# Optimization experiments

Measured on AMD Instinct MI355X. Metric: run time of the kernel, lower is better.

## Reference

```python
import jax, jax.numpy as jnp
import numpy as np

N = 50000        # n_nodes
E = 800000       # n_edges (avg degree 16)
H = 64           # hidden_size
ALPHA = 0.5      # CRF alpha
BETA = 0.5       # CRF beta
N_LAYER = 2      # args.crf_layer
GAMMA = 0.2      # LeakyReLU negative slope


def setup_inputs() -> dict:
    key = jax.random.key(0)
    k = jax.random.split(key, 5)
    emb = jax.random.normal(k[0], (N, H), jnp.float32)
    W_fc = jax.random.normal(k[1], (H, H), jnp.float32) / np.sqrt(H)
    attn_fc_w = jax.random.normal(k[2], (1, 2 * H), jnp.float32) / np.sqrt(2 * H)
    src = jax.random.randint(k[3], (E,), 0, N, dtype=jnp.int32)
    dst = jax.random.randint(k[4], (E,), 0, N, dtype=jnp.int32)
    return {"emb": emb, "W_fc": W_fc, "attn_fc_w": attn_fc_w, "src": src, "dst": dst}


def _segment_softmax(e, dst, n):
    # softmax over incoming edges of each destination node (DGL mailbox softmax)
    m = jax.ops.segment_max(e, dst, num_segments=n)
    m = jnp.where(jnp.isfinite(m), m, 0.0)  # nodes with no in-edges
    ex = jnp.exp(e - m[dst])
    denom = jax.ops.segment_sum(ex, dst, num_segments=n)
    return ex / jnp.maximum(denom[dst], 1e-16)


def reference(emb, W_fc, attn_fc_w, src, dst):
    # attn_fc(concat(z_src, z_dst)) split into two per-node projections
    a_src = attn_fc_w[0, :H]
    a_dst = attn_fc_w[0, H:]
    h = emb
    e = None
    for _ in range(N_LAYER):
        z = h @ W_fc.T                              # [N, H] emb_attn
        e = (z @ a_src)[src] + (z @ a_dst)[dst]     # [E] edge logits
        e = jnp.where(e > 0, e, GAMMA * e)          # LeakyReLU(gamma)
        att = _segment_softmax(e, dst, N)           # [E]
        crf = jax.ops.segment_sum(att[:, None] * h[src], dst, num_segments=N)  # [N, H]
        h = (ALPHA * emb + BETA * crf) / (ALPHA + BETA)
    # training loss (is_train=True); reuses last layer's edge logits e
    loss_a = jnp.sum((h - emb) ** 2, axis=-1)                     # [N]
    att = _segment_softmax(e, dst, N)
    diff = jnp.sqrt(jnp.sum((h[dst] - h[src]) ** 2, axis=-1) + 1e-12)  # [E] L2 norm
    loss_b = jax.ops.segment_sum(att * diff, dst, num_segments=N)  # [N]
    loss = jnp.mean(ALPHA * loss_a + BETA * loss_b)
    return h, loss
```

## Files before the change

kernel.cpp:

```cpp
#include <hip/hip_runtime.h>

#define NNODES 50000
#define NEDGES 800000
#define HDIM 64
#define CAP 64
#define GAMMA 0.2f
#define SCAN_B 256
#define SCAN_NB ((NNODES + SCAN_B - 1) / SCAN_B)
#define LOSS_GRID 2048
#define NPART 8
#define NODES_PER_PART ((NNODES + NPART - 1) / NPART)
#define FILL_SLICES 192
#define E4 (NEDGES / 4)
#define CHUNK ((E4 + FILL_SLICES - 1) / FILL_SLICES)

typedef unsigned short u16;
typedef unsigned int u32;

__device__ __forceinline__ u16 f2bf(float f) {
    u32 u = __float_as_uint(f);
    u32 r = (u + 0x7FFFu + ((u >> 16) & 1u)) >> 16;
    return (u16)r;
}
__device__ __forceinline__ float bflo(u32 u) { return __uint_as_float(u << 16); }
__device__ __forceinline__ float bfhi(u32 u) { return __uint_as_float(u & 0xFFFF0000u); }

__device__ __forceinline__ float wave_sum(float v) {
    #pragma unroll
    for (int off = 32; off; off >>= 1) v += __shfl_xor(v, off, 64);
    return v;
}
__device__ __forceinline__ float wave_max(float v) {
    #pragma unroll
    for (int off = 32; off; off >>= 1) v = fmaxf(v, __shfl_xor(v, off, 64));
    return v;
}
__device__ __forceinline__ int wave_sum_i(int v) {
    #pragma unroll
    for (int off = 32; off; off >>= 1) v += __shfl_xor(v, off, 64);
    return v;
}
__device__ __forceinline__ float group8_sum(float v) {
    v += __shfl_xor(v, 1, 64);
    v += __shfl_xor(v, 2, 64);
    v += __shfl_xor(v, 4, 64);
    return v;
}

__global__ void k_wswd(const float* __restrict__ Wfc, const float* __restrict__ attn,
                       float* __restrict__ ws, float* __restrict__ wd) {
    int t = threadIdx.x;
    int k = t & 63;
    const float* av = attn + ((t >= 64) ? HDIM : 0);
    float s = 0.f;
    for (int j = 0; j < HDIM; ++j) s += Wfc[j * HDIM + k] * av[j];
    if (t < 64) ws[k] = s; else wd[k] = s;
}

__global__ __launch_bounds__(256) void k_fillx(const int4* __restrict__ src4,
                                               const int4* __restrict__ dst4,
                                               int* __restrict__ cursor,
                                               u16* __restrict__ padded,
                                               const float* __restrict__ emb,
                                               const float* __restrict__ ws,
                                               const float* __restrict__ wd,
                                               u16* __restrict__ emb_bf,
                                               float* __restrict__ zs, float* __restrict__ zd) {
    if (blockIdx.x < NPART * FILL_SLICES) {
        const int part = blockIdx.x & (NPART - 1);
        const int slice = blockIdx.x >> 3;
        const int lo = slice * CHUNK;
        const int hi = min(lo + CHUNK, E4);
        const int plo = part * NODES_PER_PART;
        const int phi = plo + NODES_PER_PART;
        for (int i = lo + threadIdx.x; i < hi; i += 256) {
            int4 s = src4[i];
            int4 d = dst4[i];
            if (d.x >= plo && d.x < phi) { int p0 = atomicAdd(&cursor[d.x], 1); if (p0 < CAP) padded[d.x * CAP + p0] = (u16)s.x; }
            if (d.y >= plo && d.y < phi) { int p1 = atomicAdd(&cursor[d.y], 1); if (p1 < CAP) padded[d.y * CAP + p1] = (u16)s.y; }
            if (d.z >= plo && d.z < phi) { int p2 = atomicAdd(&cursor[d.z], 1); if (p2 < CAP) padded[d.z * CAP + p2] = (u16)s.z; }
            if (d.w >= plo && d.w < phi) { int p3 = atomicAdd(&cursor[d.w], 1); if (p3 < CAP) padded[d.w * CAP + p3] = (u16)s.w; }
        }
    }
    int tid = blockIdx.x * blockDim.x + threadIdx.x;
    int wid = tid >> 6;
    int lane = tid & 63;
    if (wid < NNODES) {
        float v = emb[wid * HDIM + lane];
        emb_bf[wid * HDIM + lane] = f2bf(v);
        float a = wave_sum(v * ws[lane]);
        float b = wave_sum(v * wd[lane]);
        if (lane == 0) { zs[wid] = a; zd[wid] = b; }
    }
}

__global__ __launch_bounds__(SCAN_B) void k_scan1(const int* __restrict__ deg,
                                                  int* __restrict__ blockSums) {
    int t = threadIdx.x;
    int idx = blockIdx.x * SCAN_B + t;
    int v = (idx < NNODES) ? min(deg[idx], CAP) : 0;
    int ws = wave_sum_i(v);
    __shared__ int part[4];
    if ((t & 63) == 0) part[t >> 6] = ws;
    __syncthreads();
    if (t == 0) blockSums[blockIdx.x] = part[0] + part[1] + part[2] + part[3];
}

__global__ __launch_bounds__(SCAN_B) void k_scan2(int* __restrict__ blockSums,
                                                  int* __restrict__ blockOffs) {
    __shared__ int s[SCAN_B];
    int t = threadIdx.x;
    int v = (t < SCAN_NB) ? blockSums[t] : 0;
    s[t] = v;
    __syncthreads();
    for (int off = 1; off < SCAN_B; off <<= 1) {
        int x = (t >= off) ? s[t - off] : 0;
        __syncthreads();
        s[t] += x;
        __syncthreads();
    }
    if (t < SCAN_NB) blockOffs[t] = s[t] - v;
}

__global__ __launch_bounds__(SCAN_B) void k_scan3(const int* __restrict__ deg,
                                                  const int* __restrict__ blockOffs,
                                                  int* __restrict__ row_ptr) {
    __shared__ int s[SCAN_B];
    int t = threadIdx.x;
    int idx = blockIdx.x * SCAN_B + t;
    int v = (idx < NNODES) ? min(deg[idx], CAP) : 0;
    s[t] = v;
    __syncthreads();
    for (int off = 1; off < SCAN_B; off <<= 1) {
        int x = (t >= off) ? s[t - off] : 0;
        __syncthreads();
        s[t] += x;
        __syncthreads();
    }
    if (idx < NNODES) {
        int excl = s[t] - v + blockOffs[blockIdx.x];
        row_ptr[idx] = excl;
        if (idx == NNODES - 1) row_ptr[NNODES] = excl + v;
    }
}

template <bool STORE_ATT, bool COMPUTE_Z, bool WRITE_F32, bool STORE_LA, bool COMPACT>
__global__ __launch_bounds__(256) void k_layer(const u16* __restrict__ hbf_in,
                                               const float* __restrict__ emb,
                                               const int* __restrict__ deg,
                                               const int* __restrict__ row_ptr,
                                               const u16* __restrict__ padded,
                                               const float* __restrict__ zs,
                                               const float* __restrict__ zd,
                                               float* __restrict__ att_csr,
                                               u16* __restrict__ csr_c,
                                               u16* __restrict__ dmap_c,
                                               float* __restrict__ h_out,
                                               u16* __restrict__ hbf_out,
                                               const float* __restrict__ ws,
                                               const float* __restrict__ wd,
                                               float* __restrict__ zs_out,
                                               float* __restrict__ zd_out,
                                               float* __restrict__ la) {
    int wid = (blockIdx.x * blockDim.x + threadIdx.x) >> 6;
    int lane = threadIdx.x & 63;
    if (wid >= NNODES) return;
    int ne = min(deg[wid], CAP);
    int s0 = 0;
    if (STORE_ATT || COMPACT) s0 = row_ptr[wid];
    float zdn = zd[wid];
    const int sub8 = lane >> 3, q8 = lane & 7;
    float acc[8];
    #pragma unroll
    for (int i = 0; i < 8; ++i) acc[i] = 0.f;

    int s = 0; float e = -INFINITY;
    bool valid = lane < ne;
    if (valid) {
        s = padded[wid * CAP + lane];
        float z = zs[s] + zdn;
        e = z > 0.f ? z : GAMMA * z;
    }
    float m = wave_max(e);
    float ex = valid ? __expf(e - m) : 0.f;
    float dsum = wave_sum(ex);
    float inv = 1.f / fmaxf(dsum, 1e-16f);
    if (STORE_ATT && valid) att_csr[s0 + lane] = ex * inv;
    if (COMPACT && valid) {
        csr_c[s0 + lane] = (u16)s;
        dmap_c[s0 + lane] = (u16)wid;
    }
    for (int j = 0; j < ne; j += 16) {
        int ja = j + sub8, jb = j + 8 + sub8;
        float wa = __shfl(ex, ja, 64);
        float wb = __shfl(ex, jb, 64);
        int ta = __shfl(s, ja, 64);
        int tb = __shfl(s, jb, 64);
        const uint4 ra = *(const uint4*)&hbf_in[(size_t)ta * HDIM + 8 * q8];
        const uint4 rb = *(const uint4*)&hbf_in[(size_t)tb * HDIM + 8 * q8];
        acc[0] += wa * bflo(ra.x) + wb * bflo(rb.x);
        acc[1] += wa * bfhi(ra.x) + wb * bfhi(rb.x);
        acc[2] += wa * bflo(ra.y) + wb * bflo(rb.y);
        acc[3] += wa * bfhi(ra.y) + wb * bfhi(rb.y);
        acc[4] += wa * bflo(ra.z) + wb * bflo(rb.z);
        acc[5] += wa * bfhi(ra.z) + wb * bfhi(rb.z);
        acc[6] += wa * bflo(ra.w) + wb * bflo(rb.w);
        acc[7] += wa * bfhi(ra.w) + wb * bfhi(rb.w);
    }
    #pragma unroll
    for (int off = 8; off <= 32; off <<= 1) {
        #pragma unroll
        for (int i = 0; i < 8; ++i) acc[i] += __shfl_xor(acc[i], off, 64);
    }
    float hv[8];
    #pragma unroll
    for (int i = 0; i < 8; ++i) hv[i] = 0.f;
    float lap = 0.f;
    if (sub8 == 0) {
        const float4 e0 = *(const float4*)&emb[(size_t)wid * HDIM + 8 * q8];
        const float4 e1 = *(const float4*)&emb[(size_t)wid * HDIM + 8 * q8 + 4];
        hv[0] = 0.5f * (e0.x + acc[0] * inv);
        hv[1] = 0.5f * (e0.y + acc[1] * inv);
        hv[2] = 0.5f * (e0.z + acc[2] * inv);
        hv[3] = 0.5f * (e0.w + acc[3] * inv);
        hv[4] = 0.5f * (e1.x + acc[4] * inv);
        hv[5] = 0.5f * (e1.y + acc[5] * inv);
        hv[6] = 0.5f * (e1.z + acc[6] * inv);
        hv[7] = 0.5f * (e1.w + acc[7] * inv);
        if (WRITE_F32) {
            *(float4*)&h_out[(size_t)wid * HDIM + 8 * q8]     = make_float4(hv[0], hv[1], hv[2], hv[3]);
            *(float4*)&h_out[(size_t)wid * HDIM + 8 * q8 + 4] = make_float4(hv[4], hv[5], hv[6], hv[7]);
        }
        uint4 o;
        o.x = (u32)f2bf(hv[0]) | ((u32)f2bf(hv[1]) << 16);
        o.y = (u32)f2bf(hv[2]) | ((u32)f2bf(hv[3]) << 16);
        o.z = (u32)f2bf(hv[4]) | ((u32)f2bf(hv[5]) << 16);
        o.w = (u32)f2bf(hv[6]) | ((u32)f2bf(hv[7]) << 16);
        *(uint4*)&hbf_out[(size_t)wid * HDIM + 8 * q8] = o;
        if (STORE_LA) {
            float d0 = hv[0] - e0.x, d1 = hv[1] - e0.y, d2 = hv[2] - e0.z, d3 = hv[3] - e0.w;
            float d4 = hv[4] - e1.x, d5 = hv[5] - e1.y, d6 = hv[6] - e1.z, d7 = hv[7] - e1.w;
            lap = d0 * d0 + d1 * d1 + d2 * d2 + d3 * d3 +
                  d4 * d4 + d5 * d5 + d6 * d6 + d7 * d7;
        }
    }
    if (STORE_LA) {
        float lsum = wave_sum(lap);
        if (lane == 0) la[wid] = lsum;
    }
    if (COMPUTE_Z) {
        float pa = 0.f, pb = 0.f;
        if (sub8 == 0) {
            const float4 w0 = *(const float4*)&ws[8 * q8];
            const float4 w1 = *(const float4*)&ws[8 * q8 + 4];
            const float4 d0 = *(const float4*)&wd[8 * q8];
            const float4 d1 = *(const float4*)&wd[8 * q8 + 4];
            pa = hv[0] * w0.x + hv[1] * w0.y + hv[2] * w0.z + hv[3] * w0.w +
                 hv[4] * w1.x + hv[5] * w1.y + hv[6] * w1.z + hv[7] * w1.w;
            pb = hv[0] * d0.x + hv[1] * d0.y + hv[2] * d0.z + hv[3] * d0.w +
                 hv[4] * d1.x + hv[5] * d1.y + hv[6] * d1.z + hv[7] * d1.w;
        }
        float a = wave_sum(pa);
        float b = wave_sum(pb);
        if (lane == 0) { zs_out[wid] = a; zd_out[wid] = b; }
    }
}

__global__ __launch_bounds__(256) void k_loss(const float* __restrict__ la,
                                              const u16* __restrict__ hbf,
                                              const u16* __restrict__ csr_src,
                                              const u16* __restrict__ dst_map,
                                              const float* __restrict__ att_csr,
                                              float* __restrict__ acc) {
    const int lane = threadIdx.x & 63;
    const int wib = threadIdx.x >> 6;
    const int gtid = blockIdx.x * blockDim.x + threadIdx.x;
    const int nthreads = gridDim.x * blockDim.x;
    const int gw = gtid >> 6;
    const int nwaves = nthreads >> 6;
    const int sub8 = lane >> 3, q8 = lane & 7;
    float lb = 0.f;

    for (int i = gtid; i < NNODES / 4; i += nthreads) {
        const float4 v = *(const float4*)&la[i * 4];
        lb += 0.5f * (v.x + v.y + v.z + v.w);
    }
    if ((NNODES & 3) != 0 && gtid < (NNODES & 3)) lb += 0.5f * la[(NNODES & ~3) + gtid];

    for (int g = gw; g < NEDGES / 16; g += nwaves) {
        int e0 = g * 16 + sub8;
        int e1 = e0 + 8;
        int s0i = csr_src[e0], d0i = dst_map[e0];
        int s1i = csr_src[e1], d1i = dst_map[e1];
        const uint4 rs0 = *(const uint4*)&hbf[(size_t)s0i * HDIM + 8 * q8];
        const uint4 rd0 = *(const uint4*)&hbf[(size_t)d0i * HDIM + 8 * q8];
        const uint4 rs1 = *(const uint4*)&hbf[(size_t)s1i * HDIM + 8 * q8];
        const uint4 rd1 = *(const uint4*)&hbf[(size_t)d1i * HDIM + 8 * q8];
        float a0 = bflo(rd0.x) - bflo(rs0.x), a1 = bfhi(rd0.x) - bfhi(rs0.x);
        float a2 = bflo(rd0.y) - bflo(rs0.y), a3 = bfhi(rd0.y) - bfhi(rs0.y);
        float a4 = bflo(rd0.z) - bflo(rs0.z), a5 = bfhi(rd0.z) - bfhi(rs0.z);
        float a6 = bflo(rd0.w) - bflo(rs0.w), a7 = bfhi(rd0.w) - bfhi(rs0.w);
        float b0 = bflo(rd1.x) - bflo(rs1.x), b1 = bfhi(rd1.x) - bfhi(rs1.x);
        float b2 = bflo(rd1.y) - bflo(rs1.y), b3 = bfhi(rd1.y) - bfhi(rs1.y);
        float b4 = bflo(rd1.z) - bflo(rs1.z), b5 = bfhi(rd1.z) - bfhi(rs1.z);
        float b6 = bflo(rd1.w) - bflo(rs1.w), b7 = bfhi(rd1.w) - bfhi(rs1.w);
        float ss0 = group8_sum(a0 * a0 + a1 * a1 + a2 * a2 + a3 * a3 +
                               a4 * a4 + a5 * a5 + a6 * a6 + a7 * a7);
        float ss1 = group8_sum(b0 * b0 + b1 * b1 + b2 * b2 + b3 * b3 +
                               b4 * b4 + b5 * b5 + b6 * b6 + b7 * b7);
        if (q8 == 0)
            lb += 0.5f * (att_csr[e0] * sqrtf(ss0 + 1e-12f) +
                          att_csr[e1] * sqrtf(ss1 + 1e-12f));
    }
    lb = wave_sum(lb);
    __shared__ float part[4];
    if (lane == 0) part[wib] = lb;
    __syncthreads();
    if (threadIdx.x == 0)
        atomicAdd(acc, part[0] + part[1] + part[2] + part[3]);
}

__global__ void k_finalize(const float* __restrict__ acc, float* __restrict__ out_loss) {
    out_loss[0] = acc[0] / (float)NNODES;
}

extern "C" void kernel_launch(void* const* d_in, const int* in_sizes, int n_in,
                              void* d_out, int out_size, void* d_ws, size_t ws_size,
                              hipStream_t stream) {
    const float* emb  = (const float*)d_in[0];
    const float* Wfc  = (const float*)d_in[1];
    const float* attn = (const float*)d_in[2];
    const int*   src  = (const int*)d_in[3];
    const int*   dst  = (const int*)d_in[4];
    float* out = (float*)d_out;

    char* p = (char*)d_ws;
    int*   cursor  = (int*)p;   p += (size_t)NNODES * 4;
    float* lossAcc = (float*)p; p += 256;
    int*   row_ptr = (int*)p;   p += (size_t)(NNODES + 1) * 4;
    int*   bsums   = (int*)p;   p += (size_t)SCAN_NB * 4;
    int*   boffs   = (int*)p;   p += (size_t)SCAN_NB * 4;
    float* wsv     = (float*)p; p += 64 * 4;
    float* wdv     = (float*)p; p += 64 * 4;
    float* zs0     = (float*)p; p += (size_t)NNODES * 4;
    float* zd0     = (float*)p; p += (size_t)NNODES * 4;
    float* zs1     = (float*)p; p += (size_t)NNODES * 4;
    float* zd1     = (float*)p; p += (size_t)NNODES * 4;
    float* laArr   = (float*)p; p += (size_t)NNODES * 4;
    float* att_csr = (float*)p; p += (size_t)NEDGES * 4;
    p = (char*)(((size_t)p + 255) & ~(size_t)255);
    u16*   padded  = (u16*)p;   p += (size_t)NNODES * CAP * 2;
    u16*   csr_src = (u16*)p;   p += (size_t)NEDGES * 2;
    u16*   dst_map = (u16*)p;   p += (size_t)NEDGES * 2;
    u16*   emb_bf  = (u16*)p;   p += (size_t)NNODES * HDIM * 2;
    u16*   h1_bf   = (u16*)p;   p += (size_t)NNODES * HDIM * 2;
    u16*   out_bf  = (u16*)p;   p += (size_t)NNODES * HDIM * 2;

    hipMemsetAsync(cursor, 0, (size_t)NNODES * 4 + 256, stream);

    const int NB = (NNODES + 3) / 4;

    k_wswd<<<1, 128, 0, stream>>>(Wfc, attn, wsv, wdv);
    k_fillx<<<NB, 256, 0, stream>>>((const int4*)src, (const int4*)dst, cursor, padded,
                                    emb, wsv, wdv, emb_bf, zs0, zd0);
    k_scan1<<<SCAN_NB, SCAN_B, 0, stream>>>(cursor, bsums);
    k_scan2<<<1, SCAN_B, 0, stream>>>(bsums, boffs);
    k_scan3<<<SCAN_NB, SCAN_B, 0, stream>>>(cursor, boffs, row_ptr);

    k_layer<false, true, false, false, true><<<NB, 256, 0, stream>>>(
        emb_bf, emb, cursor, row_ptr, padded, zs0, zd0,
        att_csr, csr_src, dst_map, out , h1_bf, wsv, wdv, zs1, zd1, laArr);
    k_layer<true, false, true, true, false><<<NB, 256, 0, stream>>>(
        h1_bf, emb, cursor, row_ptr, padded, zs1, zd1,
        att_csr, csr_src, dst_map, out, out_bf, wsv, wdv, zs0, zd0, laArr);

    k_loss<<<LOSS_GRID, 256, 0, stream>>>(laArr, out_bf, csr_src, dst_map, att_csr, lossAcc);
    k_finalize<<<1, 1, 0, stream>>>(lossAcc, out + (size_t)NNODES * HDIM);
}
```

Baseline: 231.0 us.

## Bucket edges by destination partition before scattering into padded adjacency

Building the padded adjacency used to read the full src/dst edge arrays once per each of 8 destination partitions, with most lanes filtering edges out. Now a bucketing kernel reads the edges once and packs (src,dst) pairs into per-wave, per-partition regions using ballot/popcount ranking. A scatter kernel then does the atomic inserts, keeping partition = blockIdx&7, so each partition's atomics stay on a fixed group of blocks. The emb bf16 conversion and z projections move into a fused scan1 kernel. This trades the redundant edge reads for an extra 3.2 MB intermediate write/read and one more kernel launch.

```diff
diff --git a/kernel.cpp b/kernel.cpp
--- a/kernel.cpp
+++ b/kernel.cpp
@@ -9,13 +9,15 @@
 #define SCAN_NB ((NNODES + SCAN_B - 1) / SCAN_B)
 #define LOSS_GRID 2048
 #define NPART 8
-#define NODES_PER_PART ((NNODES + NPART - 1) / NPART)
-#define FILL_SLICES 192
+#define PART_DIV 6272
 #define E4 (NEDGES / 4)
-#define CHUNK ((E4 + FILL_SLICES - 1) / FILL_SLICES)
+#define NWAVES_B1 512
+#define CHUNK_W ((E4 + NWAVES_B1 - 1) / NWAVES_B1)
+#define BCAP 512
 
 typedef unsigned short u16;
 typedef unsigned int u32;
+typedef unsigned long long u64;
 
 __device__ __forceinline__ u16 f2bf(float f) {
     u32 u = __float_as_uint(f);
@@ -57,30 +59,83 @@
     if (t < 64) ws[k] = s; else wd[k] = s;
 }
 
-__global__ __launch_bounds__(256) void k_fillx(const int4* __restrict__ src4,
-                                               const int4* __restrict__ dst4,
-                                               int* __restrict__ cursor,
-                                               u16* __restrict__ padded,
-                                               const float* __restrict__ emb,
-                                               const float* __restrict__ ws,
-                                               const float* __restrict__ wd,
-                                               u16* __restrict__ emb_bf,
-                                               float* __restrict__ zs, float* __restrict__ zd) {
-    if (blockIdx.x < NPART * FILL_SLICES) {
-        const int part = blockIdx.x & (NPART - 1);
-        const int slice = blockIdx.x >> 3;
-        const int lo = slice * CHUNK;
-        const int hi = min(lo + CHUNK, E4);
-        const int plo = part * NODES_PER_PART;
-        const int phi = plo + NODES_PER_PART;
-        for (int i = lo + threadIdx.x; i < hi; i += 256) {
-            int4 s = src4[i];
-            int4 d = dst4[i];
-            if (d.x >= plo && d.x < phi) { int p0 = atomicAdd(&cursor[d.x], 1); if (p0 < CAP) padded[d.x * CAP + p0] = (u16)s.x; }
-            if (d.y >= plo && d.y < phi) { int p1 = atomicAdd(&cursor[d.y], 1); if (p1 < CAP) padded[d.y * CAP + p1] = (u16)s.y; }
-            if (d.z >= plo && d.z < phi) { int p2 = atomicAdd(&cursor[d.z], 1); if (p2 < CAP) padded[d.z * CAP + p2] = (u16)s.z; }
-            if (d.w >= plo && d.w < phi) { int p3 = atomicAdd(&cursor[d.w], 1); if (p3 < CAP) padded[d.w * CAP + p3] = (u16)s.w; }
+__global__ __launch_bounds__(256) void k_bucket(const int4* __restrict__ src4,
+                                                const int4* __restrict__ dst4,
+                                                u32* __restrict__ region,
+                                                int* __restrict__ cnt_out) {
+    const int wid = (blockIdx.x * blockDim.x + threadIdx.x) >> 6;
+    const int lane = threadIdx.x & 63;
+    const u64 below = ((lane == 63) ? ~0ull : ((1ull << (lane + 1)) - 1)) >> 1;
+    const int lo = wid * CHUNK_W;
+    const int hi = min(lo + CHUNK_W, E4);
+    int cur[NPART];
+    #pragma unroll
+    for (int p = 0; p < NPART; ++p) cur[p] = 0;
+
+    for (int base = lo; base < hi; base += 64) {
+        int i = base + lane;
+        bool have = i < hi;
+        int4 s4 = have ? src4[i] : make_int4(0, 0, 0, 0);
+        int4 d4 = have ? dst4[i] : make_int4(0, 0, 0, 0);
+        #pragma unroll
+        for (int k = 0; k < 4; ++k) {
+            int s = (k == 0) ? s4.x : (k == 1) ? s4.y : (k == 2) ? s4.z : s4.w;
+            int d = (k == 0) ? d4.x : (k == 1) ? d4.y : (k == 2) ? d4.z : d4.w;
+            int part = have ? (d / PART_DIV) : NPART;
+            u32 v = (u32)s | ((u32)d << 16);
+            #pragma unroll
+            for (int p = 0; p < NPART; ++p) {
+                u64 m = __ballot(part == p);
+                if (m == 0ull) continue;
+                if (part == p) {
+                    int rank = __popcll(m & below);
+                    int pos = cur[p] + rank;
+                    if (pos < BCAP) region[((size_t)wid * NPART + p) * BCAP + pos] = v;
+                }
+                cur[p] += __popcll(m);
+            }
         }
+    }
+    #pragma unroll
+    for (int p = 0; p < NPART; ++p)
+        if (lane == p) cnt_out[wid * NPART + p] = min(cur[p], BCAP);
+}
+
+__global__ __launch_bounds__(256) void k_scatter(const u32* __restrict__ region,
+                                                 const int* __restrict__ cnt,
+                                                 int* __restrict__ cursor,
+                                                 u16* __restrict__ padded) {
+    const int part = blockIdx.x & (NPART - 1);
+    const int j = blockIdx.x >> 3;
+    for (int w = j; w < NWAVES_B1; w += 64) {
+        int n = cnt[w * NPART + part];
+        const u32* base = &region[((size_t)w * NPART + part) * BCAP];
+        for (int i = threadIdx.x; i < n; i += 256) {
+            u32 v = base[i];
+            int d = (int)(v >> 16);
+            int s = (int)(v & 0xFFFFu);
+            int pos = atomicAdd(&cursor[d], 1);
+            if (pos < CAP) padded[(size_t)d * CAP + pos] = (u16)s;
+        }
+    }
+}
+
+__global__ __launch_bounds__(256) void k_scan1z(const int* __restrict__ deg,
+                                                int* __restrict__ blockSums,
+                                                const float* __restrict__ emb,
+                                                const float* __restrict__ ws,
+                                                const float* __restrict__ wd,
+                                                u16* __restrict__ emb_bf,
+                                                float* __restrict__ zs, float* __restrict__ zd) {
+    int t = threadIdx.x;
+    if (blockIdx.x < SCAN_NB) {
+        int idx = blockIdx.x * SCAN_B + t;
+        int v = (idx < NNODES) ? min(deg[idx], CAP) : 0;
+        int wsum = wave_sum_i(v);
+        __shared__ int part[4];
+        if ((t & 63) == 0) part[t >> 6] = wsum;
+        __syncthreads();
+        if (t == 0) blockSums[blockIdx.x] = part[0] + part[1] + part[2] + part[3];
     }
     int tid = blockIdx.x * blockDim.x + threadIdx.x;
     int wid = tid >> 6;
@@ -92,18 +147,6 @@
         float b = wave_sum(v * wd[lane]);
         if (lane == 0) { zs[wid] = a; zd[wid] = b; }
     }
-}
-
-__global__ __launch_bounds__(SCAN_B) void k_scan1(const int* __restrict__ deg,
-                                                  int* __restrict__ blockSums) {
-    int t = threadIdx.x;
-    int idx = blockIdx.x * SCAN_B + t;
-    int v = (idx < NNODES) ? min(deg[idx], CAP) : 0;
-    int ws = wave_sum_i(v);
-    __shared__ int part[4];
-    if ((t & 63) == 0) part[t >> 6] = ws;
-    __syncthreads();
-    if (t == 0) blockSums[blockIdx.x] = part[0] + part[1] + part[2] + part[3];
 }
 
 __global__ __launch_bounds__(SCAN_B) void k_scan2(int* __restrict__ blockSums,
@@ -177,7 +220,7 @@
     int s = 0; float e = -INFINITY;
     bool valid = lane < ne;
     if (valid) {
-        s = padded[wid * CAP + lane];
+        s = padded[(size_t)wid * CAP + lane];
         float z = zs[s] + zdn;
         e = z > 0.f ? z : GAMMA * z;
     }
@@ -340,6 +383,7 @@
     int*   row_ptr = (int*)p;   p += (size_t)(NNODES + 1) * 4;
     int*   bsums   = (int*)p;   p += (size_t)SCAN_NB * 4;
     int*   boffs   = (int*)p;   p += (size_t)SCAN_NB * 4;
+    int*   bcnt    = (int*)p;   p += (size_t)NWAVES_B1 * NPART * 4;
     float* wsv     = (float*)p; p += 64 * 4;
     float* wdv     = (float*)p; p += 64 * 4;
     float* zs0     = (float*)p; p += (size_t)NNODES * 4;
@@ -349,6 +393,7 @@
     float* laArr   = (float*)p; p += (size_t)NNODES * 4;
     float* att_csr = (float*)p; p += (size_t)NEDGES * 4;
     p = (char*)(((size_t)p + 255) & ~(size_t)255);
+    u32*   region  = (u32*)p;   p += (size_t)NWAVES_B1 * NPART * BCAP * 4;
     u16*   padded  = (u16*)p;   p += (size_t)NNODES * CAP * 2;
     u16*   csr_src = (u16*)p;   p += (size_t)NEDGES * 2;
     u16*   dst_map = (u16*)p;   p += (size_t)NEDGES * 2;
@@ -361,9 +406,10 @@
     const int NB = (NNODES + 3) / 4;
 
     k_wswd<<<1, 128, 0, stream>>>(Wfc, attn, wsv, wdv);
-    k_fillx<<<NB, 256, 0, stream>>>((const int4*)src, (const int4*)dst, cursor, padded,
-                                    emb, wsv, wdv, emb_bf, zs0, zd0);
-    k_scan1<<<SCAN_NB, SCAN_B, 0, stream>>>(cursor, bsums);
+    k_bucket<<<NWAVES_B1 / 4, 256, 0, stream>>>((const int4*)src, (const int4*)dst,
+                                                region, bcnt);
+    k_scatter<<<NPART * 64, 256, 0, stream>>>(region, bcnt, cursor, padded);
+    k_scan1z<<<NB, 256, 0, stream>>>(cursor, bsums, emb, wsv, wdv, emb_bf, zs0, zd0);
     k_scan2<<<1, SCAN_B, 0, stream>>>(bsums, boffs);
     k_scan3<<<SCAN_NB, SCAN_B, 0, stream>>>(cursor, boffs, row_ptr);
 
```

Measured after the change: 250.5 us. 1.08x slower.
